# Performance work log

Hardware: AMD Instinct MI355X
Metric: run time of the kernel (lower is better)

## Reference

```python
import jax, jax.numpy as jnp
import numpy as np

B, S, D, H = 2, 2048, 1024, 16
DEPTH = D // H

def setup_inputs() -> dict:
    key = jax.random.key(0)
    ks = jax.random.split(key, 11)
    def glorot(k, shape):
        lim = np.sqrt(6.0 / (shape[0] + shape[1]))
        return jax.random.uniform(k, shape, jnp.float32, -lim, lim)
    return {
        'q': jax.random.normal(ks[0], (B, S, D), jnp.float32),
        'k': jax.random.normal(ks[1], (B, S, D), jnp.float32),
        'v': jax.random.normal(ks[2], (B, S, D), jnp.float32),
        'wq': glorot(ks[3], (D, D)), 'bq': jnp.zeros((D,), jnp.float32),
        'wk': glorot(ks[4], (D, D)), 'bk': jnp.zeros((D,), jnp.float32),
        'wv': glorot(ks[5], (D, D)), 'bv': jnp.zeros((D,), jnp.float32),
        'wo': glorot(ks[6], (D, D)), 'bo': jnp.zeros((D,), jnp.float32),
    }

def _split_heads(x):
    # [B,S,D] -> [B,H,S,depth]
    return x.reshape(B, S, H, DEPTH).transpose(0, 2, 1, 3)

def reference(q, k, v, wq, bq, wk, bk, wv, bv, wo, bo):
    qh = _split_heads(q @ wq + bq)
    kh = _split_heads(k @ wk + bk)
    vh = _split_heads(v @ wv + bv)
    scale = 1.0 / jnp.sqrt(jnp.float32(DEPTH))
    scores = jnp.einsum('bhqd,bhkd->bhqk', qh, kh) * scale
    attn = jax.nn.softmax(scores, axis=-1)
    out = jnp.einsum('bhqk,bhkd->bhqd', attn, vh)  # [B,H,S,depth]
    out = out.transpose(0, 2, 1, 3).reshape(B, S, D)
    return out @ wo + bo
```

## Files before the change

### kernel.cpp

```cpp
#include <hip/hip_runtime.h>
#include <hip/hip_bf16.h>
#include <stdint.h>

#define Bb 2
#define Ss 2048
#define Dd 1024
#define Hh 16

typedef __hip_bfloat16 bf16;
typedef __attribute__((ext_vector_type(8))) short bf16x8;
typedef __attribute__((ext_vector_type(4))) short short4v;
typedef __attribute__((ext_vector_type(4))) float f32x4;
typedef __attribute__((ext_vector_type(4))) unsigned uint4v;
typedef __attribute__((ext_vector_type(2))) unsigned uint2v;

__device__ __forceinline__ void gl_lds16(const void* g, void* l) {
  __builtin_amdgcn_global_load_lds((const __attribute__((address_space(1))) void*)g,
                                   (__attribute__((address_space(3))) void*)l, 16, 0, 0);
}

__device__ __forceinline__ unsigned pack2(float a, float b) {
  unsigned ua = __builtin_bit_cast(unsigned, a), ub = __builtin_bit_cast(unsigned, b);
  return ((ua + 0x8000u) >> 16) | ((ub + 0x8000u) & 0xffff0000u);
}

__device__ __forceinline__ bf16x8 lds_frag(const char* base, int row, int cl) {
  int phys = cl ^ (row & 7);
  return *(const bf16x8*)(base + row * 128 + phys * 16);
}

__global__ void convert_qk(const float* __restrict__ q, const float* __restrict__ k,
                           bf16* __restrict__ Qb, bf16* __restrict__ Kb) {
  int sel = blockIdx.x >> 11;
  const float* src = sel ? k : q;
  bf16* dst = sel ? Kb : Qb;
  size_t i = (size_t)(blockIdx.x & 2047) * 256 + threadIdx.x;
  f32x4 v0 = *(const f32x4*)(src + i * 8);
  f32x4 v1 = *(const f32x4*)(src + i * 8 + 4);
  uint4v o = {pack2(v0[0], v0[1]), pack2(v0[2], v0[3]),
              pack2(v1[0], v1[1]), pack2(v1[2], v1[3])};
  *(uint4v*)((char*)dst + i * 16) = o;
}

__global__ void transpose_w4(const float* w0, const float* w1, const float* w2, const float* w3,
                             bf16* t0, bf16* t1, bf16* t2, bf16* t3) {
  const float* W;
  bf16* T;
  switch (blockIdx.z) {
    case 0: W = w0; T = t0; break;
    case 1: W = w1; T = t1; break;
    case 2: W = w2; T = t2; break;
    default: W = w3; T = t3; break;
  }
  __shared__ bf16 tile[64][65];
  int tx = threadIdx.x, ty = threadIdx.y;
  int r0 = blockIdx.y * 64, c0 = blockIdx.x * 64;
#pragma unroll
  for (int j = 0; j < 16; j++) {
    int r = ty + j * 4;
    tile[r][tx] = __float2bfloat16(W[(size_t)(r0 + r) * 1024 + c0 + tx]);
  }
  __syncthreads();
#pragma unroll
  for (int j = 0; j < 16; j++) {
    int r = ty + j * 4;
    T[(size_t)(c0 + r) * 1024 + r0 + tx] = tile[tx][r];
  }
}

#define SCL 0.180336878f
__global__ __launch_bounds__(256, 3) void gemm_qkv(
    const bf16* __restrict__ Qb, const bf16* __restrict__ Kb, const float* __restrict__ v,
    const bf16* __restrict__ WTall,
    const float* __restrict__ bq, const float* __restrict__ bk, const float* __restrict__ bv,
    bf16* __restrict__ Qp, bf16* __restrict__ Kp, bf16* __restrict__ Vt) {
  __shared__ char As[128 * 128], Bs[128 * 128];
  const int K = 1024;
  int tid = threadIdx.x, lane = tid & 63, w = tid >> 6;
  int quad = lane >> 4, l16 = lane & 15;
  int xcd = blockIdx.x & 7, slot = blockIdx.x >> 3;
  int pair = xcd * 12 + (slot % 12);
  int nloc_blk = slot / 12;
  int mblk = pair / 3, sel = pair % 3;
  int m0 = mblk * 128;
  int nloc0 = nloc_blk * 128;
  int n0 = sel * 1024 + nloc0;
  const bf16* Ab = (sel == 0) ? Qb : Kb;
  const float* bias = (sel == 0) ? bq : (sel == 1) ? bk : bv;
  int wm = (w >> 1) * 64, wn = (w & 1) * 64;
  f32x4 acc[4][4] = {};
  for (int k0 = 0; k0 < K; k0 += 64) {
    __syncthreads();
    if (sel < 2) {
#pragma unroll
      for (int i = 0; i < 4; i++) {
        int c = i * 256 + tid;
        int row = c >> 3, cc = c & 7;
        int g = (cc ^ (row & 7)) * 16;
        gl_lds16((const char*)Ab + ((size_t)(m0 + row) * K + k0) * 2 + g, As + c * 16);
        gl_lds16((const char*)WTall + ((size_t)(n0 + row) * K + k0) * 2 + g, Bs + c * 16);
      }
    } else {
#pragma unroll
      for (int i = 0; i < 4; i++) {
        int c = i * 256 + tid;
        int row = c >> 3, cc = c & 7;
        int g = cc ^ (row & 7);
        const float* src = v + (size_t)(m0 + row) * K + k0 + g * 8;
        f32x4 v0 = *(const f32x4*)src;
        f32x4 v1 = *(const f32x4*)(src + 4);
        uint4v o = {pack2(v0[0], v0[1]), pack2(v0[2], v0[3]),
                    pack2(v1[0], v1[1]), pack2(v1[2], v1[3])};
        *(uint4v*)(As + c * 16) = o;
        gl_lds16((const char*)WTall + ((size_t)(n0 + row) * K + k0) * 2 + g * 16, Bs + c * 16);
      }
    }
    __syncthreads();
#pragma unroll
    for (int ks = 0; ks < 2; ks++) {
      bf16x8 a[4], b[4];
#pragma unroll
      for (int mt = 0; mt < 4; mt++) a[mt] = lds_frag(As, wm + mt * 16 + l16, ks * 4 + quad);
#pragma unroll
      for (int nt = 0; nt < 4; nt++) b[nt] = lds_frag(Bs, wn + nt * 16 + l16, ks * 4 + quad);
#pragma unroll
      for (int mt = 0; mt < 4; mt++)
#pragma unroll
        for (int nt = 0; nt < 4; nt++)
          acc[mt][nt] = __builtin_amdgcn_mfma_f32_16x16x32_bf16(a[mt], b[nt], acc[mt][nt], 0, 0, 0);
    }
  }
#pragma unroll
  for (int nt = 0; nt < 4; nt++) {
    int nloc = nloc0 + wn + nt * 16 + l16;
    float bvv = bias[nloc];
#pragma unroll
    for (int mt = 0; mt < 4; mt++) {
      int row = m0 + wm + mt * 16 + quad * 4;
      if (sel == 2) {
        int d = nloc & 63, h = nloc >> 6;
        int b_ = row >> 11, s = row & 2047;
        int bh = b_ * 16 + h;
        float f0 = acc[mt][nt][0] + bvv, f1 = acc[mt][nt][1] + bvv;
        float f2 = acc[mt][nt][2] + bvv, f3 = acc[mt][nt][3] + bvv;
        uint2v pv = {pack2(f0, f1), pack2(f2, f3)};
        *(uint2v*)((char*)Vt + ((size_t)(bh * 64 + d) * Ss + s) * 2) = pv;
      } else {
        bf16* C = (sel == 0) ? Qp : Kp;
        float scale = (sel == 0) ? SCL : 1.0f;
#pragma unroll
        for (int r = 0; r < 4; r++)
          C[(size_t)(row + r) * 1024 + nloc] = __float2bfloat16((acc[mt][nt][r] + bvv) * scale);
      }
    }
  }
}

__global__ __launch_bounds__(512, 4) void flash_attn(
    const bf16* __restrict__ Q, const bf16* __restrict__ Kp,
    const bf16* __restrict__ Vt, bf16* __restrict__ O) {
  __shared__ char lds[48 * 1024];
  int tid = threadIdx.x, lane = tid & 63, w = tid >> 6;
  int quad = lane >> 4, l16 = lane & 15;
  int bx = blockIdx.x;
  int bh = bx & 31, b = bh >> 4, h = bh & 15;
  int q0 = (bx >> 5) * 128;
  int qw = (w & 3) * 32;
  int parity = w >> 2;
  const char* Ksb = lds + 16 * 1024 + parity * 16 * 1024;
  const char* Vsb = Ksb + 8 * 1024;

#pragma unroll
  for (int i = 0; i < 2; i++) {
    int c = i * 512 + tid;
    int row = c >> 3, cc = c & 7;
    int gcol = (cc ^ (row & 7)) * 16;
    gl_lds16((const char*)Q + ((size_t)(b * Ss + q0 + row) * Dd + h * 64) * 2 + gcol, lds + c * 16);
  }

  f32x4 o_acc[2][4] = {};
  f32x4 l_acc[2] = {};
  const short4v ones4 = {(short)0x3F80, (short)0x3F80, (short)0x3F80, (short)0x3F80};

  for (int kb0 = 0; kb0 < Ss / 64; kb0 += 2) {
    __syncthreads();
    {
      int row = tid >> 3, cc = tid & 7;
      int gcol = (cc ^ (row & 7)) * 16;
#pragma unroll
      for (int i = 0; i < 4; i++) {
        int kbb = kb0 + (i >> 1);
        char* dst = lds + 16 * 1024 + i * 8 * 1024 + tid * 16;
        if ((i & 1) == 0)
          gl_lds16((const char*)Kp + ((size_t)(b * Ss + kbb * 64 + row) * Dd + h * 64) * 2 + gcol, dst);
        else
          gl_lds16((const char*)Vt + ((size_t)(bh * 64 + row) * Ss + kbb * 64) * 2 + gcol, dst);
      }
    }
    __syncthreads();

    f32x4 s[4][2] = {};
#pragma unroll
    for (int ks = 0; ks < 2; ks++) {
      bf16x8 ak[4], bq[2];
#pragma unroll
      for (int kt = 0; kt < 4; kt++) ak[kt] = lds_frag(Ksb, kt * 16 + l16, ks * 4 + quad);
#pragma unroll
      for (int qt = 0; qt < 2; qt++) bq[qt] = lds_frag(lds, qw + qt * 16 + l16, ks * 4 + quad);
#pragma unroll
      for (int kt = 0; kt < 4; kt++)
#pragma unroll
        for (int qt = 0; qt < 2; qt++)
          s[kt][qt] = __builtin_amdgcn_mfma_f32_16x16x32_bf16(ak[kt], bq[qt], s[kt][qt], 0, 0, 0);
    }

#pragma unroll
    for (int kt = 0; kt < 4; kt++) {
      short4v af[2];
#pragma unroll
      for (int qt = 0; qt < 2; qt++) {
        union { short4v s4; uint2v u2; } u;
        u.u2[0] = pack2(exp2f(s[kt][qt][0]), exp2f(s[kt][qt][1]));
        u.u2[1] = pack2(exp2f(s[kt][qt][2]), exp2f(s[kt][qt][3]));
        af[qt] = u.s4;
      }
#pragma unroll
      for (int nt = 0; nt < 4; nt++) {
        int row = nt * 16 + l16;
        int chunk = kt * 2 + (quad >> 1);
        int addr = row * 128 + ((chunk ^ (row & 7)) * 16) + (quad & 1) * 8;
        short4v bfv = *(const short4v*)(Vsb + addr);
#pragma unroll
        for (int qt = 0; qt < 2; qt++)
          o_acc[qt][nt] = __builtin_amdgcn_mfma_f32_16x16x16bf16_1k(af[qt], bfv, o_acc[qt][nt], 0, 0, 0);
      }
#pragma unroll
      for (int qt = 0; qt < 2; qt++)
        l_acc[qt] = __builtin_amdgcn_mfma_f32_16x16x16bf16_1k(af[qt], ones4, l_acc[qt], 0, 0, 0);
    }
  }

  __syncthreads();
  float* Obuf = (float*)lds;
  float* Lbuf = (float*)(lds + 32 * 1024);
  if (parity == 1) {
#pragma unroll
    for (int qt = 0; qt < 2; qt++)
#pragma unroll
      for (int r = 0; r < 4; r++) {
        int qrow = qw + qt * 16 + quad * 4 + r;
#pragma unroll
        for (int nt = 0; nt < 4; nt++) Obuf[qrow * 64 + nt * 16 + l16] = o_acc[qt][nt][r];
        Lbuf[qrow] = l_acc[qt][r];
      }
  }
  __syncthreads();
  if (parity == 0) {
#pragma unroll
    for (int qt = 0; qt < 2; qt++)
#pragma unroll
      for (int r = 0; r < 4; r++) {
        int qrow = qw + qt * 16 + quad * 4 + r;
        float inv = 1.0f / (l_acc[qt][r] + Lbuf[qrow]);
        int grow = b * Ss + q0 + qrow;
#pragma unroll
        for (int nt = 0; nt < 4; nt++) {
          float val = (o_acc[qt][nt][r] + Obuf[qrow * 64 + nt * 16 + l16]) * inv;
          O[(size_t)grow * Dd + h * 64 + nt * 16 + l16] = __float2bfloat16(val);
        }
      }
  }
}

__global__ __launch_bounds__(256, 4) void gemm_out(
    const bf16* __restrict__ AO, const bf16* __restrict__ WT,
    const float* __restrict__ bo, float* __restrict__ out) {
  __shared__ char As[64 * 128], Bs[64 * 128];
  const int K = 1024;
  int tid = threadIdx.x, lane = tid & 63, w = tid >> 6;
  int quad = lane >> 4, l16 = lane & 15;
  int xcd = blockIdx.x & 7, slot = blockIdx.x >> 3;
  int mblk = xcd * 8 + (slot & 7);
  int nblk = slot >> 3;
  int m0 = mblk * 64, n0 = nblk * 64;
  int wm = (w & 1) * 32, wn = (w >> 1) * 32;
  f32x4 acc[2][2] = {};
  for (int k0 = 0; k0 < K; k0 += 64) {
    __syncthreads();
#pragma unroll
    for (int i = 0; i < 2; i++) {
      int c = i * 256 + tid;
      int row = c >> 3, cc = c & 7;
      int g = (cc ^ (row & 7)) * 16;
      gl_lds16((const char*)AO + ((size_t)(m0 + row) * K + k0) * 2 + g, As + c * 16);
      gl_lds16((const char*)WT + ((size_t)(n0 + row) * K + k0) * 2 + g, Bs + c * 16);
    }
    __syncthreads();
#pragma unroll
    for (int ks = 0; ks < 2; ks++) {
      bf16x8 a[2], b[2];
#pragma unroll
      for (int mt = 0; mt < 2; mt++) a[mt] = lds_frag(As, wm + mt * 16 + l16, ks * 4 + quad);
#pragma unroll
      for (int nt = 0; nt < 2; nt++) b[nt] = lds_frag(Bs, wn + nt * 16 + l16, ks * 4 + quad);
#pragma unroll
      for (int mt = 0; mt < 2; mt++)
#pragma unroll
        for (int nt = 0; nt < 2; nt++)
          acc[mt][nt] = __builtin_amdgcn_mfma_f32_16x16x32_bf16(a[mt], b[nt], acc[mt][nt], 0, 0, 0);
    }
  }
#pragma unroll
  for (int nt = 0; nt < 2; nt++) {
    int col = n0 + wn + nt * 16 + l16;
    float bvv = bo[col];
#pragma unroll
    for (int mt = 0; mt < 2; mt++) {
      int row = m0 + wm + mt * 16 + quad * 4;
#pragma unroll
      for (int r = 0; r < 4; r++)
        out[(size_t)(row + r) * 1024 + col] = acc[mt][nt][r] + bvv;
    }
  }
}

extern "C" void kernel_launch(void* const* d_in, const int* in_sizes, int n_in,
                              void* d_out, int out_size, void* d_ws, size_t ws_size,
                              hipStream_t stream) {
  const float* q  = (const float*)d_in[0];
  const float* k  = (const float*)d_in[1];
  const float* v  = (const float*)d_in[2];
  const float* wq = (const float*)d_in[3];
  const float* bq = (const float*)d_in[4];
  const float* wk = (const float*)d_in[5];
  const float* bk = (const float*)d_in[6];
  const float* wv = (const float*)d_in[7];
  const float* bv = (const float*)d_in[8];
  const float* wo = (const float*)d_in[9];
  const float* bo = (const float*)d_in[10];
  float* out = (float*)d_out;

  char* ws = (char*)d_ws;
  const size_t MB = (size_t)1024 * 1024;
  bf16* wtall = (bf16*)(ws + 0 * MB);
  bf16* wtq = wtall;
  bf16* wtk = (bf16*)(ws + 2 * MB);
  bf16* wtv = (bf16*)(ws + 4 * MB);
  bf16* wto = (bf16*)(ws + 6 * MB);
  bf16* Qp  = (bf16*)(ws + 8 * MB);
  bf16* AO  = Qp;
  bf16* Kp  = (bf16*)(ws + 16 * MB);
  bf16* Vt  = (bf16*)(ws + 24 * MB);
  bf16* Qb  = (bf16*)((char*)d_out + 0 * MB);
  bf16* Kb  = (bf16*)((char*)d_out + 8 * MB);

  dim3 tb(64, 4);
  convert_qk<<<4096, 256, 0, stream>>>(q, k, Qb, Kb);
  transpose_w4<<<dim3(16, 16, 4), tb, 0, stream>>>(wq, wk, wv, wo, wtq, wtk, wtv, wto);
  gemm_qkv<<<768, 256, 0, stream>>>(Qb, Kb, v, wtall, bq, bk, bv, Qp, Kp, Vt);
  flash_attn<<<512, 512, 0, stream>>>(Qp, Kp, Vt, AO);
  gemm_out<<<1024, 256, 0, stream>>>(AO, wto, bo, out);
}
```

Before: 245.0 us.

## Drop LDS staging in flash attention and fuse prep kernels

Flash attention now has each wave own 16 query rows and load K and V fragments directly from global memory into registers. This replaces the shared LDS tiles, the block barriers and the two-parity split-K merge. The convert and weight-transpose kernels are merged into one launch. This removes LDS and sync overhead and one launch, but it multiplies global/L2 reads of K and V because tiles are no longer shared across waves, and it leaves load latency unhidden.

```diff
diff --git a/kernel.cpp b/kernel.cpp
--- a/kernel.cpp
+++ b/kernel.cpp
@@ -29,42 +29,46 @@
   return *(const bf16x8*)(base + row * 128 + phys * 16);
 }
 
-__global__ void convert_qk(const float* __restrict__ q, const float* __restrict__ k,
-                           bf16* __restrict__ Qb, bf16* __restrict__ Kb) {
-  int sel = blockIdx.x >> 11;
-  const float* src = sel ? k : q;
-  bf16* dst = sel ? Kb : Qb;
-  size_t i = (size_t)(blockIdx.x & 2047) * 256 + threadIdx.x;
-  f32x4 v0 = *(const f32x4*)(src + i * 8);
-  f32x4 v1 = *(const f32x4*)(src + i * 8 + 4);
-  uint4v o = {pack2(v0[0], v0[1]), pack2(v0[2], v0[3]),
-              pack2(v1[0], v1[1]), pack2(v1[2], v1[3])};
-  *(uint4v*)((char*)dst + i * 16) = o;
-}
-
-__global__ void transpose_w4(const float* w0, const float* w1, const float* w2, const float* w3,
-                             bf16* t0, bf16* t1, bf16* t2, bf16* t3) {
-  const float* W;
-  bf16* T;
-  switch (blockIdx.z) {
-    case 0: W = w0; T = t0; break;
-    case 1: W = w1; T = t1; break;
-    case 2: W = w2; T = t2; break;
-    default: W = w3; T = t3; break;
-  }
+__global__ void prep(const float* __restrict__ q, const float* __restrict__ k,
+                     const float* w0, const float* w1, const float* w2, const float* w3,
+                     bf16* __restrict__ Qb, bf16* __restrict__ Kb,
+                     bf16* t0, bf16* t1, bf16* t2, bf16* t3) {
   __shared__ bf16 tile[64][65];
-  int tx = threadIdx.x, ty = threadIdx.y;
-  int r0 = blockIdx.y * 64, c0 = blockIdx.x * 64;
-#pragma unroll
-  for (int j = 0; j < 16; j++) {
-    int r = ty + j * 4;
-    tile[r][tx] = __float2bfloat16(W[(size_t)(r0 + r) * 1024 + c0 + tx]);
-  }
-  __syncthreads();
-#pragma unroll
-  for (int j = 0; j < 16; j++) {
-    int r = ty + j * 4;
-    T[(size_t)(c0 + r) * 1024 + r0 + tx] = tile[tx][r];
+  int bx = blockIdx.x;
+  if (bx < 4096) {
+    int sel = bx >> 11;
+    const float* src = sel ? k : q;
+    bf16* dst = sel ? Kb : Qb;
+    size_t i = (size_t)(bx & 2047) * 256 + threadIdx.x;
+    f32x4 v0 = *(const f32x4*)(src + i * 8);
+    f32x4 v1 = *(const f32x4*)(src + i * 8 + 4);
+    uint4v o = {pack2(v0[0], v0[1]), pack2(v0[2], v0[3]),
+                pack2(v1[0], v1[1]), pack2(v1[2], v1[3])};
+    *(uint4v*)((char*)dst + i * 16) = o;
+  } else {
+    int rem = bx - 4096;
+    int bz = rem >> 8, by = (rem >> 4) & 15, bxx = rem & 15;
+    const float* W;
+    bf16* T;
+    switch (bz) {
+      case 0: W = w0; T = t0; break;
+      case 1: W = w1; T = t1; break;
+      case 2: W = w2; T = t2; break;
+      default: W = w3; T = t3; break;
+    }
+    int tx = threadIdx.x & 63, ty = threadIdx.x >> 6;
+    int r0 = by * 64, c0 = bxx * 64;
+#pragma unroll
+    for (int j = 0; j < 16; j++) {
+      int r = ty + j * 4;
+      tile[r][tx] = __float2bfloat16(W[(size_t)(r0 + r) * 1024 + c0 + tx]);
+    }
+    __syncthreads();
+#pragma unroll
+    for (int j = 0; j < 16; j++) {
+      int r = ty + j * 4;
+      T[(size_t)(c0 + r) * 1024 + r0 + tx] = tile[tx][r];
+    }
   }
 }
 
@@ -156,119 +160,62 @@
   }
 }
 
-__global__ __launch_bounds__(512, 4) void flash_attn(
+__global__ __launch_bounds__(256, 4) void flash_attn(
     const bf16* __restrict__ Q, const bf16* __restrict__ Kp,
     const bf16* __restrict__ Vt, bf16* __restrict__ O) {
-  __shared__ char lds[48 * 1024];
   int tid = threadIdx.x, lane = tid & 63, w = tid >> 6;
   int quad = lane >> 4, l16 = lane & 15;
   int bx = blockIdx.x;
   int bh = bx & 31, b = bh >> 4, h = bh & 15;
-  int q0 = (bx >> 5) * 128;
-  int qw = (w & 3) * 32;
-  int parity = w >> 2;
-  const char* Ksb = lds + 16 * 1024 + parity * 16 * 1024;
-  const char* Vsb = Ksb + 8 * 1024;
-
-#pragma unroll
-  for (int i = 0; i < 2; i++) {
-    int c = i * 512 + tid;
-    int row = c >> 3, cc = c & 7;
-    int gcol = (cc ^ (row & 7)) * 16;
-    gl_lds16((const char*)Q + ((size_t)(b * Ss + q0 + row) * Dd + h * 64) * 2 + gcol, lds + c * 16);
-  }
-
-  f32x4 o_acc[2][4] = {};
-  f32x4 l_acc[2] = {};
+  int qbase = (bx >> 5) * 64 + w * 16;
+
+  const bf16* Kbase = Kp + (size_t)b * Ss * Dd + h * 64;
+  const bf16* Vbase = Vt + (size_t)bh * 64 * Ss;
+
+  bf16x8 qf[2];
+#pragma unroll
+  for (int ks = 0; ks < 2; ks++)
+    qf[ks] = *(const bf16x8*)(Q + (size_t)(b * Ss + qbase + l16) * Dd + h * 64 + ks * 32 + quad * 8);
+
+  f32x4 o_acc[4] = {};
+  f32x4 l_acc = {};
   const short4v ones4 = {(short)0x3F80, (short)0x3F80, (short)0x3F80, (short)0x3F80};
 
-  for (int kb0 = 0; kb0 < Ss / 64; kb0 += 2) {
-    __syncthreads();
-    {
-      int row = tid >> 3, cc = tid & 7;
-      int gcol = (cc ^ (row & 7)) * 16;
-#pragma unroll
-      for (int i = 0; i < 4; i++) {
-        int kbb = kb0 + (i >> 1);
-        char* dst = lds + 16 * 1024 + i * 8 * 1024 + tid * 16;
-        if ((i & 1) == 0)
-          gl_lds16((const char*)Kp + ((size_t)(b * Ss + kbb * 64 + row) * Dd + h * 64) * 2 + gcol, dst);
-        else
-          gl_lds16((const char*)Vt + ((size_t)(bh * 64 + row) * Ss + kbb * 64) * 2 + gcol, dst);
-      }
-    }
-    __syncthreads();
-
-    f32x4 s[4][2] = {};
-#pragma unroll
-    for (int ks = 0; ks < 2; ks++) {
-      bf16x8 ak[4], bq[2];
-#pragma unroll
-      for (int kt = 0; kt < 4; kt++) ak[kt] = lds_frag(Ksb, kt * 16 + l16, ks * 4 + quad);
-#pragma unroll
-      for (int qt = 0; qt < 2; qt++) bq[qt] = lds_frag(lds, qw + qt * 16 + l16, ks * 4 + quad);
-#pragma unroll
-      for (int kt = 0; kt < 4; kt++)
-#pragma unroll
-        for (int qt = 0; qt < 2; qt++)
-          s[kt][qt] = __builtin_amdgcn_mfma_f32_16x16x32_bf16(ak[kt], bq[qt], s[kt][qt], 0, 0, 0);
-    }
-
+#pragma unroll 2
+  for (int kb = 0; kb < Ss / 64; kb++) {
+    f32x4 s[4] = {};
+#pragma unroll
+    for (int kt = 0; kt < 4; kt++)
+#pragma unroll
+      for (int ks = 0; ks < 2; ks++) {
+        bf16x8 ak = *(const bf16x8*)(Kbase + (size_t)(kb * 64 + kt * 16 + l16) * Dd +
+                                     ks * 32 + quad * 8);
+        s[kt] = __builtin_amdgcn_mfma_f32_16x16x32_bf16(ak, qf[ks], s[kt], 0, 0, 0);
+      }
 #pragma unroll
     for (int kt = 0; kt < 4; kt++) {
-      short4v af[2];
-#pragma unroll
-      for (int qt = 0; qt < 2; qt++) {
-        union { short4v s4; uint2v u2; } u;
-        u.u2[0] = pack2(exp2f(s[kt][qt][0]), exp2f(s[kt][qt][1]));
-        u.u2[1] = pack2(exp2f(s[kt][qt][2]), exp2f(s[kt][qt][3]));
-        af[qt] = u.s4;
-      }
+      union { short4v s4; uint2v u2; } u;
+      u.u2[0] = pack2(exp2f(s[kt][0]), exp2f(s[kt][1]));
+      u.u2[1] = pack2(exp2f(s[kt][2]), exp2f(s[kt][3]));
+      short4v af = u.s4;
 #pragma unroll
       for (int nt = 0; nt < 4; nt++) {
-        int row = nt * 16 + l16;
-        int chunk = kt * 2 + (quad >> 1);
-        int addr = row * 128 + ((chunk ^ (row & 7)) * 16) + (quad & 1) * 8;
-        short4v bfv = *(const short4v*)(Vsb + addr);
-#pragma unroll
-        for (int qt = 0; qt < 2; qt++)
-          o_acc[qt][nt] = __builtin_amdgcn_mfma_f32_16x16x16bf16_1k(af[qt], bfv, o_acc[qt][nt], 0, 0, 0);
-      }
-#pragma unroll
-      for (int qt = 0; qt < 2; qt++)
-        l_acc[qt] = __builtin_amdgcn_mfma_f32_16x16x16bf16_1k(af[qt], ones4, l_acc[qt], 0, 0, 0);
-    }
-  }
-
-  __syncthreads();
-  float* Obuf = (float*)lds;
-  float* Lbuf = (float*)(lds + 32 * 1024);
-  if (parity == 1) {
-#pragma unroll
-    for (int qt = 0; qt < 2; qt++)
-#pragma unroll
-      for (int r = 0; r < 4; r++) {
-        int qrow = qw + qt * 16 + quad * 4 + r;
-#pragma unroll
-        for (int nt = 0; nt < 4; nt++) Obuf[qrow * 64 + nt * 16 + l16] = o_acc[qt][nt][r];
-        Lbuf[qrow] = l_acc[qt][r];
-      }
-  }
-  __syncthreads();
-  if (parity == 0) {
-#pragma unroll
-    for (int qt = 0; qt < 2; qt++)
-#pragma unroll
-      for (int r = 0; r < 4; r++) {
-        int qrow = qw + qt * 16 + quad * 4 + r;
-        float inv = 1.0f / (l_acc[qt][r] + Lbuf[qrow]);
-        int grow = b * Ss + q0 + qrow;
-#pragma unroll
-        for (int nt = 0; nt < 4; nt++) {
-          float val = (o_acc[qt][nt][r] + Obuf[qrow * 64 + nt * 16 + l16]) * inv;
-          O[(size_t)grow * Dd + h * 64 + nt * 16 + l16] = __float2bfloat16(val);
-        }
-      }
+        short4v bv = *(const short4v*)(Vbase + (size_t)(nt * 16 + l16) * Ss +
+                                       kb * 64 + kt * 16 + quad * 4);
+        o_acc[nt] = __builtin_amdgcn_mfma_f32_16x16x16bf16_1k(af, bv, o_acc[nt], 0, 0, 0);
+      }
+      l_acc = __builtin_amdgcn_mfma_f32_16x16x16bf16_1k(af, ones4, l_acc, 0, 0, 0);
+    }
+  }
+
+#pragma unroll
+  for (int r = 0; r < 4; r++) {
+    float inv = 1.0f / l_acc[r];
+    int grow = b * Ss + qbase + quad * 4 + r;
+#pragma unroll
+    for (int nt = 0; nt < 4; nt++)
+      O[(size_t)grow * Dd + h * 64 + nt * 16 + l16] =
+          __float2bfloat16(o_acc[nt][r] * inv);
   }
 }
 
@@ -354,10 +301,8 @@
   bf16* Qb  = (bf16*)((char*)d_out + 0 * MB);
   bf16* Kb  = (bf16*)((char*)d_out + 8 * MB);
 
-  dim3 tb(64, 4);
-  convert_qk<<<4096, 256, 0, stream>>>(q, k, Qb, Kb);
-  transpose_w4<<<dim3(16, 16, 4), tb, 0, stream>>>(wq, wk, wv, wo, wtq, wtk, wtv, wto);
+  prep<<<5120, 256, 0, stream>>>(q, k, wq, wk, wv, wo, Qb, Kb, wtq, wtk, wtv, wto);
   gemm_qkv<<<768, 256, 0, stream>>>(Qb, Kb, v, wtall, bq, bk, bv, Qp, Kp, Vt);
-  flash_attn<<<512, 512, 0, stream>>>(Qp, Kp, Vt, AO);
+  flash_attn<<<1024, 256, 0, stream>>>(Qp, Kp, Vt, AO);
   gemm_out<<<1024, 256, 0, stream>>>(AO, wto, bo, out);
 }
```

Result: slower. 517.6 us (+111.3%).
